# Kernel tuning notes

Hardware: AMD Instinct MI355X
Metric: run time of the kernel (lower is better)

## Reference

```python
import jax, jax.numpy as jnp
import numpy as np


def _d2(a, b):
    # squared euclidean distances, clamped at 0 (matches _full_cdist before sqrt)
    a2 = jnp.sum(a * a, axis=1)[:, None]
    b2 = jnp.sum(b * b, axis=1)[None, :]
    return jnp.clip(a2 + b2 - 2.0 * (a @ b.T), 0.0, None)


def _node_weights(pts, w1, b1, w2, b2):
    h = jax.nn.relu(pts @ w1 + b1)
    logits = h @ w2 + b2
    w = jax.nn.softplus(logits) + 1e-6
    w = w / jnp.sum(w)
    return w[:, 0]


def setup_inputs() -> dict:
    key = jax.random.key(0)
    ks = jax.random.split(key, 8)
    N, M, D, H, S = 8192, 8192, 2, 32, 3
    return {
        "base_points": jax.random.normal(ks[0], (N, D), jnp.float32),
        "target_points": jax.random.normal(ks[1], (M, D), jnp.float32),
        "log_sigmas": jnp.log(jnp.array([0.05, 0.1, 0.2], jnp.float32)),
        "log_scale": 0.1 * jax.random.normal(ks[2], (D,), jnp.float32),
        "wn_w1": jax.random.normal(ks[3], (D, H), jnp.float32) / np.sqrt(D),
        "wn_b1": jnp.zeros((H,), jnp.float32),
        "wn_w2": jax.random.normal(ks[4], (H, 1), jnp.float32) / np.sqrt(H),
        "wn_b2": jnp.zeros((1,), jnp.float32),
        "g_w1": jax.random.normal(ks[5], (4, H), jnp.float32) / 2.0,
        "g_b1": jnp.zeros((H,), jnp.float32),
        "g_w2": jax.random.normal(ks[6], (H, S), jnp.float32) / np.sqrt(H),
        "g_b2": jnp.zeros((S,), jnp.float32),
        "bias": jnp.zeros((1,), jnp.float32),
    }


def reference(base_points, target_points, log_sigmas, log_scale,
              wn_w1, wn_b1, wn_w2, wn_b2,
              g_w1, g_b1, g_w2, g_b2, bias):
    # learned anisotropic per-axis scale
    scale = jnp.exp(log_scale)
    base = base_points * scale
    target = target_points * scale

    # learned positive, normalized node weights (shared weight_net)
    w_b = _node_weights(base, wn_w1, wn_b1, wn_w2, wn_b2)
    w_t = _node_weights(target, wn_w1, wn_b1, wn_w2, wn_b2)

    # kde_mmd_loss with center=True: subtract weighted mean of each cloud.
    bc = base - jnp.sum(w_b[:, None] * base, axis=0)
    tc = target - jnp.sum(w_t[:, None] * target, axis=0)

    # squared distances computed ONCE, reused across all sigma bands
    d2_aa = _d2(bc, bc)
    d2_bb = _d2(tc, tc)
    d2_ab = _d2(bc, tc)

    sigmas = jnp.exp(log_sigmas)

    def band_loss(sigma):
        inv = 1.0 / (2.0 * sigma * sigma)
        kaa = jnp.exp(-d2_aa * inv)
        kbb = jnp.exp(-d2_bb * inv)
        kab = jnp.exp(-d2_ab * inv)
        # weighted MMD^2: w_a K_aa w_a + w_b K_bb w_b - 2 w_a K_ab w_b
        return (w_b @ (kaa @ w_b) + w_t @ (kbb @ w_t)
                - 2.0 * (w_b @ (kab @ w_t)))

    per_band = jnp.stack([band_loss(sigmas[i]) for i in range(sigmas.shape[0])])

    # gating statistics (torch.tensor([...]) detaches -> stop_gradient)
    dist = jnp.sqrt(_d2(base, target))
    mean_dist = jnp.mean(dist)
    var_dist = jnp.var(dist, ddof=1)  # torch .var() is unbiased
    n_base = base_points.shape[0]
    size_diff = abs(float(n_base - target_points.shape[0])) / (n_base + 1e-6)
    weight_var = jnp.var(w_b, ddof=1) + jnp.var(w_t, ddof=1)
    stats = jax.lax.stop_gradient(
        jnp.stack([mean_dist, var_dist,
                   jnp.asarray(size_diff, base.dtype), weight_var]))

    mix_logits = jax.nn.relu(stats @ g_w1 + g_b1) @ g_w2 + g_b2
    gw = jax.nn.softplus(mix_logits)
    gw = gw / jnp.sum(gw)
    return jnp.sum(gw * per_band) + bias[0]
```

## Files before the change

kernel.cpp:

```cpp
#include <hip/hip_runtime.h>
#include <math.h>

#define JTA 32
#define JTT 64
#define ITILE 1024
#define T8 8
#define NJOB_AB 2048
#define NJOB_TRI 576
#define NBLK (NJOB_AB + 2 * NJOB_TRI)
#define L2E 1.4426950408889634f

typedef float v2f __attribute__((ext_vector_type(2)));

__device__ inline float fexp2n(float x) {
  float r;
  asm("v_exp_f32 %0, -%1" : "=v"(r) : "v"(x));
  return r;
}
__device__ inline float fsqrt(float x) {
  float r;
  asm("v_sqrt_f32 %0, %1" : "=v"(r) : "v"(x));
  return r;
}

__device__ inline double wred_d(double v) {
#pragma unroll
  for (int o = 32; o > 0; o >>= 1) v += __shfl_down(v, o, 64);
  return v;
}

__device__ inline double bred(double v, double* sm) {
  v = wred_d(v);
  __syncthreads();
  if ((threadIdx.x & 63) == 0) sm[threadIdx.x >> 6] = v;
  __syncthreads();
  return sm[0] + sm[1] + sm[2] + sm[3];
}

__device__ inline void slot_reduce(const double* slot, double* smean, int nc) {
  if (threadIdx.x < 64) {
    int l = threadIdx.x;
    const double* sl = slot + l * 8;
    for (int c = 0; c < nc; ++c) {
      double v = sl[c];
      double vb = (l < 32) ? v : 0.0;
      double vt = (l < 32) ? 0.0 : v;
      vb = wred_d(vb);
      vt = wred_d(vt);
      if (l == 0) {
        smean[c] = vb;
        smean[8 + c] = vt;
      }
    }
  }
}

__global__ __launch_bounds__(256) void prep_kernel(
    const float* __restrict__ base, const float* __restrict__ target,
    const float* __restrict__ log_sigmas, const float* __restrict__ log_scale,
    const float* __restrict__ w1, const float* __restrict__ b1,
    const float* __restrict__ w2, const float* __restrict__ b2,
    float2* __restrict__ pxy, float* __restrict__ pu,
    double* __restrict__ slot, unsigned* __restrict__ fctr, int n) {
  __shared__ double sm[4];
  int gid = blockIdx.x * 256 + threadIdx.x;
  int isT = gid >= n;
  const float* pts = isT ? target : base;
  int idx = isT ? gid - n : gid;
  float ex = __expf(log_scale[0]);
  float ey = __expf(log_scale[1]);
  float s2 = __expf(log_sigmas[2]);
  float r2 = __fsqrt_rn(L2E / (2.f * s2 * s2));
  float2 p = ((const float2*)pts)[idx];
  float xr = p.x * ex, yr = p.y * ey;
  float logit = b2[0];
#pragma unroll
  for (int k = 0; k < 32; ++k) {
    float h = fmaf(xr, w1[k], fmaf(yr, w1[32 + k], b1[k]));
    h = fmaxf(h, 0.f);
    logit = fmaf(h, w2[k], logit);
  }
  float u = fmaxf(logit, 0.f) + log1pf(__expf(-fabsf(logit))) + 1e-6f;
  float X = xr * r2, Y = yr * r2;
  pxy[gid] = make_float2(X, Y);
  pu[gid] = u;
  double su = bred((double)u, sm);
  double qu = bred((double)u * (double)u, sm);
  double mx = bred((double)u * (double)X, sm);
  double my = bred((double)u * (double)Y, sm);
  double sx = bred((double)X, sm);
  double sy = bred((double)Y, sm);
  double sr = bred((double)X * (double)X + (double)Y * (double)Y, sm);
  if (threadIdx.x == 0) {
    double* s = slot + blockIdx.x * 8;
    s[0] = su;
    s[1] = qu;
    s[2] = mx;
    s[3] = my;
    s[4] = sx;
    s[5] = sy;
    s[6] = sr;
    s[7] = 0.0;
    if (blockIdx.x == 0) *fctr = 0u;
  }
}

template <bool AB, bool FAST>
__device__ inline void tile_loop(const float* sx, const float* sy,
                                 const float* su, const float* snb,
                                 const v2f xi2[4], const v2f yi2[4],
                                 const v2f al2[4], float rr0, float rr1,
                                 v2f a0[4], v2f a1[4], v2f a2[4], float& sdo) {
  constexpr int N2 = (AB ? JTA : JTT) / 2;
  float sda = 0.f, sdb = 0.f;
  const v2f vz = {0.f, 0.f};
#pragma unroll 2
  for (int jj = 0; jj < N2; ++jj) {
    v2f xj = *(const v2f*)&sx[2 * jj];
    v2f yj = *(const v2f*)&sy[2 * jj];
    v2f uj = *(const v2f*)&su[2 * jj];
    v2f nbj;
    if constexpr (AB) nbj = *(const v2f*)&snb[2 * jj];
#pragma unroll
    for (int i = 0; i < 4; ++i) {
      v2f dx = xi2[i] - xj;
      v2f dy = yi2[i] - yj;
      v2f pos = dx * dx + dy * dy;
      v2f k2 = {fexp2n(pos.x), fexp2n(pos.y)};
      v2f k0, k1;
      if constexpr (FAST) {
        v2f t = k2 * k2;
        k1 = t * t;
        v2f t1 = k1 * k1;
        k0 = t1 * t1;
      } else {
        v2f m1 = pos * rr1;
        v2f m0 = pos * rr0;
        k1 = {fexp2n(m1.x), fexp2n(m1.y)};
        k0 = {fexp2n(m0.x), fexp2n(m0.y)};
      }
      a0[i] += uj * k0;
      a1[i] += uj * k1;
      a2[i] += uj * k2;
      if constexpr (AB) {
        v2f anb = al2[i] + nbj;
        v2f d2u = pos + anb;
        d2u = __builtin_elementwise_max(d2u, vz);
        sda += fsqrt(d2u.x);
        sdb += fsqrt(d2u.y);
      }
    }
  }
  sdo = sda + sdb;
}

__global__ __launch_bounds__(256) void pair_kernel(
    const float2* __restrict__ pxy, const float* __restrict__ pu,
    const double* __restrict__ slot, double* __restrict__ paa,
    double* __restrict__ pbb, double* __restrict__ pab,
    double* __restrict__ psd, unsigned* __restrict__ fctr,
    const float* __restrict__ log_sigmas, const float* __restrict__ g_w1,
    const float* __restrict__ g_b1, const float* __restrict__ g_w2,
    const float* __restrict__ g_b2, const float* __restrict__ bias,
    float* __restrict__ out, int n) {
  __shared__ __align__(16) float sx[JTT];
  __shared__ __align__(16) float sy[JTT];
  __shared__ __align__(16) float su[JTT];
  __shared__ __align__(16) float snb[JTT];
  __shared__ double sm[4];
  __shared__ double smean[16];
  __shared__ int lastf;

  int b = blockIdx.x;
  int m, it, jt = 0, j0, pidx;
  if (b < NJOB_AB) {
    m = 2;
    pidx = b;
    it = b >> 8;
    j0 = (b & 255) * JTA;
  } else {
    int r = b - NJOB_AB;
    m = (r < NJOB_TRI) ? 0 : 1;
    if (m == 1) r -= NJOB_TRI;
    pidx = r;
    int tile = r >> 4;
    int q = r & 15;
    int idx = tile, len = T8;
    it = 0;
    while (idx >= len) {
      idx -= len;
      --len;
      ++it;
    }
    jt = it + idx;
    j0 = jt * ITILE + q * JTT;
  }
  const float2* pxyI = pxy + ((m == 1) ? n : 0);
  const float* puI = pu + ((m == 1) ? n : 0);
  const float2* pxyJ = pxy + ((m == 0) ? 0 : n);
  const float* puJ = pu + ((m == 0) ? 0 : n);

  float cx = 0.f, cy = 0.f, cx2 = 0.f, cy2 = 0.f, cc = 0.f;
  if (m == 2) {
    slot_reduce(slot, smean, 4);
  }

  float s0 = __expf(log_sigmas[0]);
  float s1 = __expf(log_sigmas[1]);
  float s2 = __expf(log_sigmas[2]);
  float rr0 = (s2 * s2) / (s0 * s0);
  float rr1 = (s2 * s2) / (s1 * s1);
  bool fast = (fabsf(rr0 - 16.f) <= 0.016f) && (fabsf(rr1 - 4.f) <= 0.004f);

  if (m == 2) {
    __syncthreads();
    cx = (float)(smean[2] / smean[0] - smean[10] / smean[8]);
    cy = (float)(smean[3] / smean[0] - smean[11] / smean[8]);
    cx2 = 2.f * cx;
    cy2 = 2.f * cy;
    cc = cx * cx + cy * cy;
  }

  int jcnt = (m == 2) ? JTA : JTT;
  if (threadIdx.x < jcnt) {
    float2 v = pxyJ[j0 + threadIdx.x];
    sx[threadIdx.x] = v.x;
    sy[threadIdx.x] = v.y;
    su[threadIdx.x] = puJ[j0 + threadIdx.x];
    if (m == 2) snb[threadIdx.x] = -fmaf(cx2, v.x, cy2 * v.y);
  }
  __syncthreads();

  int i0 = it * ITILE + threadIdx.x;
  v2f xi2[4], yi2[4], al2[4];
  float u[4];
#pragma unroll
  for (int i = 0; i < 4; ++i) {
    float2 P = pxyI[i0 + i * 256];
    u[i] = puI[i0 + i * 256];
    float xv = P.x, yv = P.y, alv = 0.f;
    if (m == 2) {
      xv -= cx;
      yv -= cy;
      alv = fmaf(cx2, xv, cy2 * yv) + cc;
    }
    xi2[i] = (v2f){xv, xv};
    yi2[i] = (v2f){yv, yv};
    al2[i] = (v2f){alv, alv};
  }

  v2f a0[4] = {}, a1[4] = {}, a2[4] = {};
  float sd = 0.f;
  if (m == 2) {
    if (fast)
      tile_loop<true, true>(sx, sy, su, snb, xi2, yi2, al2, rr0, rr1, a0, a1,
                            a2, sd);
    else
      tile_loop<true, false>(sx, sy, su, snb, xi2, yi2, al2, rr0, rr1, a0, a1,
                             a2, sd);
  } else {
    if (fast)
      tile_loop<false, true>(sx, sy, su, snb, xi2, yi2, al2, rr0, rr1, a0, a1,
                             a2, sd);
    else
      tile_loop<false, false>(sx, sy, su, snb, xi2, yi2, al2, rr0, rr1, a0,
                              a1, a2, sd);
  }

  double wgt = (m != 2 && jt != it) ? 2.0 : 1.0;
  double c0 = 0.0, c1 = 0.0, c2 = 0.0;
#pragma unroll
  for (int i = 0; i < 4; ++i) {
    c0 += (double)u[i] * (double)(a0[i].x + a0[i].y);
    c1 += (double)u[i] * (double)(a1[i].x + a1[i].y);
    c2 += (double)u[i] * (double)(a2[i].x + a2[i].y);
  }
  double r0 = bred(c0, sm) * wgt;
  double r1 = bred(c1, sm) * wgt;
  double r2d = bred(c2, sm) * wgt;
  double* prow = (m == 0) ? paa : (m == 1) ? pbb : pab;
  int stride = (m == 2) ? NJOB_AB : NJOB_TRI;
  if (threadIdx.x == 0) {
    prow[0 * stride + pidx] = r0;
    prow[1 * stride + pidx] = r1;
    prow[2 * stride + pidx] = r2d;
  }
  if (m == 2) {
    double rsd = bred((double)sd, sm);
    if (threadIdx.x == 0) psd[pidx] = rsd;
  }

  if (threadIdx.x == 0) {
    __threadfence();
    unsigned old = atomicAdd(fctr, 1u);
    lastf = (old == NBLK - 1) ? 1 : 0;
  }
  __syncthreads();
  if (!lastf) return;
  __threadfence();

  slot_reduce(slot, smean, 7);
  __syncthreads();
  int t = threadIdx.x;
  double vaa[3], vbb[3], vab[3];
  for (int s = 0; s < 3; ++s) {
    const double* pa = paa + s * NJOB_TRI;
    const double* pb = pbb + s * NJOB_TRI;
    const double* pc = pab + s * NJOB_AB;
    double va = pa[t] + pa[t + 256] + ((t < 64) ? pa[t + 512] : 0.0);
    double vb = pb[t] + pb[t + 256] + ((t < 64) ? pb[t + 512] : 0.0);
    double vc = 0.0;
#pragma unroll
    for (int qq = 0; qq < 8; ++qq) vc += pc[t + 256 * qq];
    vaa[s] = bred(va, sm);
    vbb[s] = bred(vb, sm);
    vab[s] = bred(vc, sm);
  }
  double sdv = 0.0;
#pragma unroll
  for (int qq = 0; qq < 8; ++qq) sdv += psd[t + 256 * qq];
  double sdt = bred(sdv, sm);

  if (threadIdx.x == 0) {
    double Sb = smean[0], Qb = smean[1], St = smean[8], Qt = smean[9];
    double SXb = smean[4], SYb = smean[5], SRb = smean[6];
    double SXt = smean[12], SYt = smean[13], SRt = smean[14];
    double pband[3];
    for (int s = 0; s < 3; ++s)
      pband[s] = vaa[s] / (Sb * Sb) + vbb[s] / (St * St) -
                 2.0 * vab[s] / (Sb * St);
    double NN = (double)n;
    double sq_sc = NN * (SRb + SRt) - 2.0 * (SXb * SXt + SYb * SYt);
    double s2d = (double)s2;
    double r2sq = (double)L2E / (2.0 * s2d * s2d);
    double sd_real = sdt / sqrt(r2sq);
    double sq_real = sq_sc / r2sq;
    double NM = NN * NN;
    double mean_d = sd_real / NM;
    double var_d = (sq_real - sd_real * sd_real / NM) / (NM - 1.0);
    double wv = (Qb / (Sb * Sb) - 1.0 / NN) / (NN - 1.0) +
                (Qt / (St * St) - 1.0 / NN) / (NN - 1.0);
    float st[4] = {(float)mean_d, (float)var_d, 0.f, (float)wv};
    float gl[3] = {g_b2[0], g_b2[1], g_b2[2]};
    for (int k = 0; k < 32; ++k) {
      float h = g_b1[k];
      for (int c = 0; c < 4; ++c) h = fmaf(st[c], g_w1[c * 32 + k], h);
      h = fmaxf(h, 0.f);
      for (int s = 0; s < 3; ++s) gl[s] = fmaf(h, g_w2[k * 3 + s], gl[s]);
    }
    float gw[3];
    float gsum = 0.f;
    for (int s = 0; s < 3; ++s) {
      gw[s] = fmaxf(gl[s], 0.f) + log1pf(__expf(-fabsf(gl[s])));
      gsum += gw[s];
    }
    double r = 0.0;
    for (int s = 0; s < 3; ++s) r += (double)(gw[s] / gsum) * pband[s];
    out[0] = (float)(r + (double)bias[0]);
  }
}

extern "C" void kernel_launch(void* const* d_in, const int* in_sizes, int n_in,
                              void* d_out, int out_size, void* d_ws,
                              size_t ws_size, hipStream_t stream) {
  const float* base = (const float*)d_in[0];
  const float* target = (const float*)d_in[1];
  const float* log_sigmas = (const float*)d_in[2];
  const float* log_scale = (const float*)d_in[3];
  const float* wn_w1 = (const float*)d_in[4];
  const float* wn_b1 = (const float*)d_in[5];
  const float* wn_w2 = (const float*)d_in[6];
  const float* wn_b2 = (const float*)d_in[7];
  const float* g_w1 = (const float*)d_in[8];
  const float* g_b1 = (const float*)d_in[9];
  const float* g_w2 = (const float*)d_in[10];
  const float* g_b2 = (const float*)d_in[11];
  const float* bias = (const float*)d_in[12];
  int n = in_sizes[0] / 2;

  double* dbase = (double*)d_ws;
  double* slot = dbase;
  double* paa = dbase + 512;
  double* pbb = paa + 3 * NJOB_TRI;
  double* pab = pbb + 3 * NJOB_TRI;
  double* psd = pab + 3 * NJOB_AB;
  double* dend = psd + NJOB_AB;
  float2* pxy = (float2*)dend;
  float* pu = (float*)(pxy + 2 * n);
  unsigned* fctr = (unsigned*)(pu + 2 * n);

  prep_kernel<<<(2 * n) / 256, 256, 0, stream>>>(
      base, target, log_sigmas, log_scale, wn_w1, wn_b1, wn_w2, wn_b2, pxy, pu,
      slot, fctr, n);
  pair_kernel<<<NBLK, 256, 0, stream>>>(pxy, pu, slot, paa, pbb, pab, psd,
                                        fctr, log_sigmas, g_w1, g_b1, g_w2,
                                        g_b2, bias, (float*)d_out, n);
}
```

Baseline: 166.0 us.

## Use persistent blocks with atomic work queue and per-block accumulated partials

Replaces the one-job-per-block launch with a fixed grid of persistent blocks that pull jobs from an atomic counter, and widens cross-tile jobs to 64 columns so they match the triangular jobs. Each block keeps scaled running sums across its jobs and writes one set of partials, which simplifies the final reduction. This aims to even out load imbalance and cut per-block reduction and launch overhead. The cost is an atomic plus a barrier per job and every block doing the slot reduction up front.

```diff
diff --git a/kernel.cpp b/kernel.cpp
--- a/kernel.cpp
+++ b/kernel.cpp
@@ -1,13 +1,13 @@
 #include <hip/hip_runtime.h>
 #include <math.h>
 
-#define JTA 32
-#define JTT 64
+#define JT 64
 #define ITILE 1024
 #define T8 8
-#define NJOB_AB 2048
+#define NJOB_AB 1024
 #define NJOB_TRI 576
-#define NBLK (NJOB_AB + 2 * NJOB_TRI)
+#define NJOB (NJOB_AB + 2 * NJOB_TRI)
+#define GRID 2048
 #define L2E 1.4426950408889634f
 
 typedef float v2f __attribute__((ext_vector_type(2)));
@@ -61,7 +61,8 @@
     const float* __restrict__ w1, const float* __restrict__ b1,
     const float* __restrict__ w2, const float* __restrict__ b2,
     float2* __restrict__ pxy, float* __restrict__ pu,
-    double* __restrict__ slot, unsigned* __restrict__ fctr, int n) {
+    double* __restrict__ slot, unsigned* __restrict__ fctr,
+    unsigned* __restrict__ qctr, int n) {
   __shared__ double sm[4];
   int gid = blockIdx.x * 256 + threadIdx.x;
   int isT = gid >= n;
@@ -101,7 +102,10 @@
     s[5] = sy;
     s[6] = sr;
     s[7] = 0.0;
-    if (blockIdx.x == 0) *fctr = 0u;
+    if (blockIdx.x == 0) {
+      *fctr = 0u;
+      *qctr = 0u;
+    }
   }
 }
 
@@ -111,11 +115,10 @@
                                  const v2f xi2[4], const v2f yi2[4],
                                  const v2f al2[4], float rr0, float rr1,
                                  v2f a0[4], v2f a1[4], v2f a2[4], float& sdo) {
-  constexpr int N2 = (AB ? JTA : JTT) / 2;
   float sda = 0.f, sdb = 0.f;
   const v2f vz = {0.f, 0.f};
 #pragma unroll 2
-  for (int jj = 0; jj < N2; ++jj) {
+  for (int jj = 0; jj < JT / 2; ++jj) {
     v2f xj = *(const v2f*)&sx[2 * jj];
     v2f yj = *(const v2f*)&sy[2 * jj];
     v2f uj = *(const v2f*)&su[2 * jj];
@@ -156,54 +159,31 @@
 
 __global__ __launch_bounds__(256) void pair_kernel(
     const float2* __restrict__ pxy, const float* __restrict__ pu,
-    const double* __restrict__ slot, double* __restrict__ paa,
-    double* __restrict__ pbb, double* __restrict__ pab,
-    double* __restrict__ psd, unsigned* __restrict__ fctr,
+    const double* __restrict__ slot, double* __restrict__ pblk,
+    unsigned* __restrict__ fctr, unsigned* __restrict__ qctr,
     const float* __restrict__ log_sigmas, const float* __restrict__ g_w1,
     const float* __restrict__ g_b1, const float* __restrict__ g_w2,
     const float* __restrict__ g_b2, const float* __restrict__ bias,
     float* __restrict__ out, int n) {
-  __shared__ __align__(16) float sx[JTT];
-  __shared__ __align__(16) float sy[JTT];
-  __shared__ __align__(16) float su[JTT];
-  __shared__ __align__(16) float snb[JTT];
+  __shared__ __align__(16) float sx[JT];
+  __shared__ __align__(16) float sy[JT];
+  __shared__ __align__(16) float su[JT];
+  __shared__ __align__(16) float snb[JT];
   __shared__ double sm[4];
   __shared__ double smean[16];
+  __shared__ int sjob;
   __shared__ int lastf;
 
-  int b = blockIdx.x;
-  int m, it, jt = 0, j0, pidx;
-  if (b < NJOB_AB) {
-    m = 2;
-    pidx = b;
-    it = b >> 8;
-    j0 = (b & 255) * JTA;
-  } else {
-    int r = b - NJOB_AB;
-    m = (r < NJOB_TRI) ? 0 : 1;
-    if (m == 1) r -= NJOB_TRI;
-    pidx = r;
-    int tile = r >> 4;
-    int q = r & 15;
-    int idx = tile, len = T8;
-    it = 0;
-    while (idx >= len) {
-      idx -= len;
-      --len;
-      ++it;
-    }
-    jt = it + idx;
-    j0 = jt * ITILE + q * JTT;
-  }
-  const float2* pxyI = pxy + ((m == 1) ? n : 0);
-  const float* puI = pu + ((m == 1) ? n : 0);
-  const float2* pxyJ = pxy + ((m == 0) ? 0 : n);
-  const float* puJ = pu + ((m == 0) ? 0 : n);
-
-  float cx = 0.f, cy = 0.f, cx2 = 0.f, cy2 = 0.f, cc = 0.f;
-  if (m == 2) {
-    slot_reduce(slot, smean, 4);
-  }
+  slot_reduce(slot, smean, 4);
+  __syncthreads();
+  double Sb = smean[0], St = smean[8];
+  float cx = (float)(smean[2] / Sb - smean[10] / St);
+  float cy = (float)(smean[3] / Sb - smean[11] / St);
+  float cx2 = 2.f * cx, cy2 = 2.f * cy;
+  float cc = cx * cx + cy * cy;
+  double sc_aa = 1.0 / (Sb * Sb);
+  double sc_bb = 1.0 / (St * St);
+  double sc_ab = -2.0 / (Sb * St);
 
   float s0 = __expf(log_sigmas[0]);
   float s1 = __expf(log_sigmas[1]);
@@ -212,88 +192,116 @@
   float rr1 = (s2 * s2) / (s1 * s1);
   bool fast = (fabsf(rr0 - 16.f) <= 0.016f) && (fabsf(rr1 - 4.f) <= 0.004f);
 
-  if (m == 2) {
+  double cacc0 = 0.0, cacc1 = 0.0, cacc2 = 0.0, sdacc = 0.0;
+  for (;;) {
+    if (threadIdx.x == 0) sjob = (int)atomicAdd(qctr, 1u);
     __syncthreads();
-    cx = (float)(smean[2] / smean[0] - smean[10] / smean[8]);
-    cy = (float)(smean[3] / smean[0] - smean[11] / smean[8]);
-    cx2 = 2.f * cx;
-    cy2 = 2.f * cy;
-    cc = cx * cx + cy * cy;
-  }
-
-  int jcnt = (m == 2) ? JTA : JTT;
-  if (threadIdx.x < jcnt) {
-    float2 v = pxyJ[j0 + threadIdx.x];
-    sx[threadIdx.x] = v.x;
-    sy[threadIdx.x] = v.y;
-    su[threadIdx.x] = puJ[j0 + threadIdx.x];
-    if (m == 2) snb[threadIdx.x] = -fmaf(cx2, v.x, cy2 * v.y);
-  }
-  __syncthreads();
-
-  int i0 = it * ITILE + threadIdx.x;
-  v2f xi2[4], yi2[4], al2[4];
-  float u[4];
-#pragma unroll
-  for (int i = 0; i < 4; ++i) {
-    float2 P = pxyI[i0 + i * 256];
-    u[i] = puI[i0 + i * 256];
-    float xv = P.x, yv = P.y, alv = 0.f;
+    int jb = sjob;
+    if (jb >= NJOB) break;
+
+    int m, it, jt = 0, j0;
+    double wgt = 1.0;
+    if (jb < NJOB_AB) {
+      m = 2;
+      it = jb >> 7;
+      j0 = (jb & 127) * JT;
+    } else {
+      int r = jb - NJOB_AB;
+      m = (r < NJOB_TRI) ? 0 : 1;
+      if (m == 1) r -= NJOB_TRI;
+      int tile = r >> 4;
+      int q = r & 15;
+      int idx = tile, len = T8;
+      it = 0;
+      while (idx >= len) {
+        idx -= len;
+        --len;
+        ++it;
+      }
+      jt = it + idx;
+      j0 = jt * ITILE + q * JT;
+      if (jt != it) wgt = 2.0;
+    }
+    const float2* pxyI = pxy + ((m == 1) ? n : 0);
+    const float* puI = pu + ((m == 1) ? n : 0);
+    const float2* pxyJ = pxy + ((m == 0) ? 0 : n);
+    const float* puJ = pu + ((m == 0) ? 0 : n);
+
+    if (threadIdx.x < JT) {
+      float2 v = pxyJ[j0 + threadIdx.x];
+      sx[threadIdx.x] = v.x;
+      sy[threadIdx.x] = v.y;
+      su[threadIdx.x] = puJ[j0 + threadIdx.x];
+      if (m == 2) snb[threadIdx.x] = -fmaf(cx2, v.x, cy2 * v.y);
+    }
+
+    int i0 = it * ITILE + threadIdx.x;
+    v2f xi2[4], yi2[4], al2[4];
+    float u[4];
+#pragma unroll
+    for (int i = 0; i < 4; ++i) {
+      float2 P = pxyI[i0 + i * 256];
+      u[i] = puI[i0 + i * 256];
+      float xv = P.x, yv = P.y, alv = 0.f;
+      if (m == 2) {
+        xv -= cx;
+        yv -= cy;
+        alv = fmaf(cx2, xv, cy2 * yv) + cc;
+      }
+      xi2[i] = (v2f){xv, xv};
+      yi2[i] = (v2f){yv, yv};
+      al2[i] = (v2f){alv, alv};
+    }
+    __syncthreads();
+
+    v2f a0[4] = {}, a1[4] = {}, a2[4] = {};
+    float sd = 0.f;
     if (m == 2) {
-      xv -= cx;
-      yv -= cy;
-      alv = fmaf(cx2, xv, cy2 * yv) + cc;
-    }
-    xi2[i] = (v2f){xv, xv};
-    yi2[i] = (v2f){yv, yv};
-    al2[i] = (v2f){alv, alv};
-  }
-
-  v2f a0[4] = {}, a1[4] = {}, a2[4] = {};
-  float sd = 0.f;
-  if (m == 2) {
-    if (fast)
-      tile_loop<true, true>(sx, sy, su, snb, xi2, yi2, al2, rr0, rr1, a0, a1,
-                            a2, sd);
-    else
-      tile_loop<true, false>(sx, sy, su, snb, xi2, yi2, al2, rr0, rr1, a0, a1,
-                             a2, sd);
-  } else {
-    if (fast)
-      tile_loop<false, true>(sx, sy, su, snb, xi2, yi2, al2, rr0, rr1, a0, a1,
-                             a2, sd);
-    else
-      tile_loop<false, false>(sx, sy, su, snb, xi2, yi2, al2, rr0, rr1, a0,
-                              a1, a2, sd);
-  }
-
-  double wgt = (m != 2 && jt != it) ? 2.0 : 1.0;
-  double c0 = 0.0, c1 = 0.0, c2 = 0.0;
-#pragma unroll
-  for (int i = 0; i < 4; ++i) {
-    c0 += (double)u[i] * (double)(a0[i].x + a0[i].y);
-    c1 += (double)u[i] * (double)(a1[i].x + a1[i].y);
-    c2 += (double)u[i] * (double)(a2[i].x + a2[i].y);
-  }
-  double r0 = bred(c0, sm) * wgt;
-  double r1 = bred(c1, sm) * wgt;
-  double r2d = bred(c2, sm) * wgt;
-  double* prow = (m == 0) ? paa : (m == 1) ? pbb : pab;
-  int stride = (m == 2) ? NJOB_AB : NJOB_TRI;
+      if (fast)
+        tile_loop<true, true>(sx, sy, su, snb, xi2, yi2, al2, rr0, rr1, a0, a1,
+                              a2, sd);
+      else
+        tile_loop<true, false>(sx, sy, su, snb, xi2, yi2, al2, rr0, rr1, a0,
+                               a1, a2, sd);
+    } else {
+      if (fast)
+        tile_loop<false, true>(sx, sy, su, snb, xi2, yi2, al2, rr0, rr1, a0,
+                               a1, a2, sd);
+      else
+        tile_loop<false, false>(sx, sy, su, snb, xi2, yi2, al2, rr0, rr1, a0,
+                                a1, a2, sd);
+    }
+
+    double jc0 = 0.0, jc1 = 0.0, jc2 = 0.0;
+#pragma unroll
+    for (int i = 0; i < 4; ++i) {
+      jc0 += (double)u[i] * (double)(a0[i].x + a0[i].y);
+      jc1 += (double)u[i] * (double)(a1[i].x + a1[i].y);
+      jc2 += (double)u[i] * (double)(a2[i].x + a2[i].y);
+    }
+    double jscale = ((m == 0) ? sc_aa : (m == 1) ? sc_bb : sc_ab) * wgt;
+    cacc0 += jscale * jc0;
+    cacc1 += jscale * jc1;
+    cacc2 += jscale * jc2;
+    if (m == 2) sdacc += (double)sd;
+  }
+
+  double r0 = bred(cacc0, sm);
+  double r1 = bred(cacc1, sm);
+  double r2d = bred(cacc2, sm);
+  double rsd = bred(sdacc, sm);
   if (threadIdx.x == 0) {
-    prow[0 * stride + pidx] = r0;
-    prow[1 * stride + pidx] = r1;
-    prow[2 * stride + pidx] = r2d;
-  }
-  if (m == 2) {
-    double rsd = bred((double)sd, sm);
-    if (threadIdx.x == 0) psd[pidx] = rsd;
+    double* p = pblk + (size_t)blockIdx.x * 4;
+    p[0] = r0;
+    p[1] = r1;
+    p[2] = r2d;
+    p[3] = rsd;
   }
 
   if (threadIdx.x == 0) {
     __threadfence();
     unsigned old = atomicAdd(fctr, 1u);
-    lastf = (old == NBLK - 1) ? 1 : 0;
+    lastf = (old == GRID - 1) ? 1 : 0;
   }
   __syncthreads();
   if (!lastf) return;
@@ -302,44 +310,36 @@
   slot_reduce(slot, smean, 7);
   __syncthreads();
   int t = threadIdx.x;
-  double vaa[3], vbb[3], vab[3];
-  for (int s = 0; s < 3; ++s) {
-    const double* pa = paa + s * NJOB_TRI;
-    const double* pb = pbb + s * NJOB_TRI;
-    const double* pc = pab + s * NJOB_AB;
-    double va = pa[t] + pa[t + 256] + ((t < 64) ? pa[t + 512] : 0.0);
-    double vb = pb[t] + pb[t + 256] + ((t < 64) ? pb[t + 512] : 0.0);
-    double vc = 0.0;
-#pragma unroll
-    for (int qq = 0; qq < 8; ++qq) vc += pc[t + 256 * qq];
-    vaa[s] = bred(va, sm);
-    vbb[s] = bred(vb, sm);
-    vab[s] = bred(vc, sm);
-  }
-  double sdv = 0.0;
-#pragma unroll
-  for (int qq = 0; qq < 8; ++qq) sdv += psd[t + 256 * qq];
-  double sdt = bred(sdv, sm);
+  double v0 = 0.0, v1 = 0.0, v2 = 0.0, vs = 0.0;
+#pragma unroll
+  for (int q = 0; q < GRID / 256; ++q) {
+    const double* p = pblk + (size_t)(t + 256 * q) * 4;
+    v0 += p[0];
+    v1 += p[1];
+    v2 += p[2];
+    vs += p[3];
+  }
+  v0 = bred(v0, sm);
+  v1 = bred(v1, sm);
+  v2 = bred(v2, sm);
+  vs = bred(vs, sm);
 
   if (threadIdx.x == 0) {
-    double Sb = smean[0], Qb = smean[1], St = smean[8], Qt = smean[9];
+    double Sb2 = smean[0], Qb = smean[1], St2 = smean[8], Qt = smean[9];
     double SXb = smean[4], SYb = smean[5], SRb = smean[6];
     double SXt = smean[12], SYt = smean[13], SRt = smean[14];
-    double pband[3];
-    for (int s = 0; s < 3; ++s)
-      pband[s] = vaa[s] / (Sb * Sb) + vbb[s] / (St * St) -
-                 2.0 * vab[s] / (Sb * St);
+    double pband[3] = {v0, v1, v2};
     double NN = (double)n;
     double sq_sc = NN * (SRb + SRt) - 2.0 * (SXb * SXt + SYb * SYt);
     double s2d = (double)s2;
     double r2sq = (double)L2E / (2.0 * s2d * s2d);
-    double sd_real = sdt / sqrt(r2sq);
+    double sd_real = vs / sqrt(r2sq);
     double sq_real = sq_sc / r2sq;
     double NM = NN * NN;
     double mean_d = sd_real / NM;
     double var_d = (sq_real - sd_real * sd_real / NM) / (NM - 1.0);
-    double wv = (Qb / (Sb * Sb) - 1.0 / NN) / (NN - 1.0) +
-                (Qt / (St * St) - 1.0 / NN) / (NN - 1.0);
+    double wv = (Qb / (Sb2 * Sb2) - 1.0 / NN) / (NN - 1.0) +
+                (Qt / (St2 * St2) - 1.0 / NN) / (NN - 1.0);
     float st[4] = {(float)mean_d, (float)var_d, 0.f, (float)wv};
     float gl[3] = {g_b2[0], g_b2[1], g_b2[2]};
     for (int k = 0; k < 32; ++k) {
@@ -380,19 +380,17 @@
 
   double* dbase = (double*)d_ws;
   double* slot = dbase;
-  double* paa = dbase + 512;
-  double* pbb = paa + 3 * NJOB_TRI;
-  double* pab = pbb + 3 * NJOB_TRI;
-  double* psd = pab + 3 * NJOB_AB;
-  double* dend = psd + NJOB_AB;
+  double* pblk = dbase + 512;
+  double* dend = pblk + GRID * 4;
   float2* pxy = (float2*)dend;
   float* pu = (float*)(pxy + 2 * n);
   unsigned* fctr = (unsigned*)(pu + 2 * n);
+  unsigned* qctr = fctr + 1;
 
   prep_kernel<<<(2 * n) / 256, 256, 0, stream>>>(
       base, target, log_sigmas, log_scale, wn_w1, wn_b1, wn_w2, wn_b2, pxy, pu,
-      slot, fctr, n);
-  pair_kernel<<<NBLK, 256, 0, stream>>>(pxy, pu, slot, paa, pbb, pab, psd,
-                                        fctr, log_sigmas, g_w1, g_b1, g_w2,
-                                        g_b2, bias, (float*)d_out, n);
-}
+      slot, fctr, qctr, n);
+  pair_kernel<<<GRID, 256, 0, stream>>>(pxy, pu, slot, pblk, fctr, qctr,
+                                        log_sigmas, g_w1, g_b1, g_w2, g_b2,
+                                        bias, (float*)d_out, n);
+}
```

Measured after the change: 181.0 us. 1.09x slower.

## Expand squared distance into dot form, widen AB tiles, batch block reductions

Applied to the files above, without the earlier changes.

The pair loop now writes the squared distance as -2*xi·xj + |xj|^2 + |xi|^2. The per-point norms are precomputed, one into shared memory and one held in registers, so each pair costs two FMAs plus an add instead of two subtracts and squares. The cross (AB) job tile is widened from 32 to 64 columns, which halves the number of AB blocks and the partial sums the final block has to gather. The four per-block reductions are fused into one pass of wavefront reductions and a single barrier instead of four serialized block reductions. The expanded distance form can lose accuracy through cancellation for nearby points, and fewer AB blocks means less parallelism.

```diff
diff --git a/kernel.cpp b/kernel.cpp
--- a/kernel.cpp
+++ b/kernel.cpp
@@ -1,11 +1,10 @@
 #include <hip/hip_runtime.h>
 #include <math.h>
 
-#define JTA 32
-#define JTT 64
+#define JT 64
 #define ITILE 1024
 #define T8 8
-#define NJOB_AB 2048
+#define NJOB_AB 1024
 #define NJOB_TRI 576
 #define NBLK (NJOB_AB + 2 * NJOB_TRI)
 #define L2E 1.4426950408889634f
@@ -107,25 +106,24 @@
 
 template <bool AB, bool FAST>
 __device__ inline void tile_loop(const float* sx, const float* sy,
-                                 const float* su, const float* snb,
-                                 const v2f xi2[4], const v2f yi2[4],
-                                 const v2f al2[4], float rr0, float rr1,
-                                 v2f a0[4], v2f a1[4], v2f a2[4], float& sdo) {
-  constexpr int N2 = (AB ? JTA : JTT) / 2;
-  float sda = 0.f, sdb = 0.f;
+                                 const float* sr, const float* su,
+                                 const float* snb, const v2f xin2[4],
+                                 const v2f yin2[4], const v2f ric2[4],
+                                 const v2f rca2[4], float rr0, float rr1,
+                                 v2f a0[4], v2f a1[4], v2f a2[4], v2f& sdv) {
   const v2f vz = {0.f, 0.f};
 #pragma unroll 2
-  for (int jj = 0; jj < N2; ++jj) {
+  for (int jj = 0; jj < JT / 2; ++jj) {
     v2f xj = *(const v2f*)&sx[2 * jj];
     v2f yj = *(const v2f*)&sy[2 * jj];
+    v2f rj = *(const v2f*)&sr[2 * jj];
     v2f uj = *(const v2f*)&su[2 * jj];
     v2f nbj;
     if constexpr (AB) nbj = *(const v2f*)&snb[2 * jj];
 #pragma unroll
     for (int i = 0; i < 4; ++i) {
-      v2f dx = xi2[i] - xj;
-      v2f dy = yi2[i] - yj;
-      v2f pos = dx * dx + dy * dy;
+      v2f core = xin2[i] * xj + (yin2[i] * yj + rj);
+      v2f pos = core + ric2[i];
       v2f k2 = {fexp2n(pos.x), fexp2n(pos.y)};
       v2f k0, k1;
       if constexpr (FAST) {
@@ -143,15 +141,13 @@
       a1[i] += uj * k1;
       a2[i] += uj * k2;
       if constexpr (AB) {
-        v2f anb = al2[i] + nbj;
-        v2f d2u = pos + anb;
+        v2f d2u = core + (rca2[i] + nbj);
         d2u = __builtin_elementwise_max(d2u, vz);
-        sda += fsqrt(d2u.x);
-        sdb += fsqrt(d2u.y);
+        v2f s = {fsqrt(d2u.x), fsqrt(d2u.y)};
+        sdv += s;
       }
     }
   }
-  sdo = sda + sdb;
 }
 
 __global__ __launch_bounds__(256) void pair_kernel(
@@ -163,11 +159,13 @@
     const float* __restrict__ g_b1, const float* __restrict__ g_w2,
     const float* __restrict__ g_b2, const float* __restrict__ bias,
     float* __restrict__ out, int n) {
-  __shared__ __align__(16) float sx[JTT];
-  __shared__ __align__(16) float sy[JTT];
-  __shared__ __align__(16) float su[JTT];
-  __shared__ __align__(16) float snb[JTT];
+  __shared__ __align__(16) float sx[JT];
+  __shared__ __align__(16) float sy[JT];
+  __shared__ __align__(16) float sr[JT];
+  __shared__ __align__(16) float su[JT];
+  __shared__ __align__(16) float snb[JT];
   __shared__ double sm[4];
+  __shared__ double smq[16];
   __shared__ double smean[16];
   __shared__ int lastf;
 
@@ -176,8 +174,8 @@
   if (b < NJOB_AB) {
     m = 2;
     pidx = b;
-    it = b >> 8;
-    j0 = (b & 255) * JTA;
+    it = b >> 7;
+    j0 = (b & 127) * JT;
   } else {
     int r = b - NJOB_AB;
     m = (r < NJOB_TRI) ? 0 : 1;
@@ -193,7 +191,7 @@
       ++it;
     }
     jt = it + idx;
-    j0 = jt * ITILE + q * JTT;
+    j0 = jt * ITILE + q * JT;
   }
   const float2* pxyI = pxy + ((m == 1) ? n : 0);
   const float* puI = pu + ((m == 1) ? n : 0);
@@ -221,18 +219,18 @@
     cc = cx * cx + cy * cy;
   }
 
-  int jcnt = (m == 2) ? JTA : JTT;
-  if (threadIdx.x < jcnt) {
+  if (threadIdx.x < JT) {
     float2 v = pxyJ[j0 + threadIdx.x];
     sx[threadIdx.x] = v.x;
     sy[threadIdx.x] = v.y;
+    sr[threadIdx.x] = fmaf(v.x, v.x, v.y * v.y);
     su[threadIdx.x] = puJ[j0 + threadIdx.x];
     if (m == 2) snb[threadIdx.x] = -fmaf(cx2, v.x, cy2 * v.y);
   }
   __syncthreads();
 
   int i0 = it * ITILE + threadIdx.x;
-  v2f xi2[4], yi2[4], al2[4];
+  v2f xin2[4], yin2[4], ric2[4], rca2[4];
   float u[4];
 #pragma unroll
   for (int i = 0; i < 4; ++i) {
@@ -244,30 +242,31 @@
       yv -= cy;
       alv = fmaf(cx2, xv, cy2 * yv) + cc;
     }
-    xi2[i] = (v2f){xv, xv};
-    yi2[i] = (v2f){yv, yv};
-    al2[i] = (v2f){alv, alv};
+    float ric = fmaf(xv, xv, yv * yv);
+    xin2[i] = (v2f){-2.f * xv, -2.f * xv};
+    yin2[i] = (v2f){-2.f * yv, -2.f * yv};
+    ric2[i] = (v2f){ric, ric};
+    rca2[i] = (v2f){ric + alv, ric + alv};
   }
 
   v2f a0[4] = {}, a1[4] = {}, a2[4] = {};
-  float sd = 0.f;
+  v2f sdv = {0.f, 0.f};
   if (m == 2) {
     if (fast)
-      tile_loop<true, true>(sx, sy, su, snb, xi2, yi2, al2, rr0, rr1, a0, a1,
-                            a2, sd);
+      tile_loop<true, true>(sx, sy, sr, su, snb, xin2, yin2, ric2, rca2, rr0,
+                            rr1, a0, a1, a2, sdv);
     else
-      tile_loop<true, false>(sx, sy, su, snb, xi2, yi2, al2, rr0, rr1, a0, a1,
-                             a2, sd);
+      tile_loop<true, false>(sx, sy, sr, su, snb, xin2, yin2, ric2, rca2, rr0,
+                             rr1, a0, a1, a2, sdv);
   } else {
     if (fast)
-      tile_loop<false, true>(sx, sy, su, snb, xi2, yi2, al2, rr0, rr1, a0, a1,
-                             a2, sd);
+      tile_loop<false, true>(sx, sy, sr, su, snb, xin2, yin2, ric2, rca2, rr0,
+                             rr1, a0, a1, a2, sdv);
     else
-      tile_loop<false, false>(sx, sy, su, snb, xi2, yi2, al2, rr0, rr1, a0,
-                              a1, a2, sd);
-  }
-
-  double wgt = (m != 2 && jt != it) ? 2.0 : 1.0;
+      tile_loop<false, false>(sx, sy, sr, su, snb, xin2, yin2, ric2, rca2, rr0,
+                              rr1, a0, a1, a2, sdv);
+  }
+
   double c0 = 0.0, c1 = 0.0, c2 = 0.0;
 #pragma unroll
   for (int i = 0; i < 4; ++i) {
@@ -275,19 +274,31 @@
     c1 += (double)u[i] * (double)(a1[i].x + a1[i].y);
     c2 += (double)u[i] * (double)(a2[i].x + a2[i].y);
   }
-  double r0 = bred(c0, sm) * wgt;
-  double r1 = bred(c1, sm) * wgt;
-  double r2d = bred(c2, sm) * wgt;
-  double* prow = (m == 0) ? paa : (m == 1) ? pbb : pab;
-  int stride = (m == 2) ? NJOB_AB : NJOB_TRI;
+  double sdd = (double)(sdv.x + sdv.y);
+  c0 = wred_d(c0);
+  c1 = wred_d(c1);
+  c2 = wred_d(c2);
+  sdd = wred_d(sdd);
+  if ((threadIdx.x & 63) == 0) {
+    double* q = &smq[(threadIdx.x >> 6) * 4];
+    q[0] = c0;
+    q[1] = c1;
+    q[2] = c2;
+    q[3] = sdd;
+  }
+  __syncthreads();
   if (threadIdx.x == 0) {
-    prow[0 * stride + pidx] = r0;
-    prow[1 * stride + pidx] = r1;
-    prow[2 * stride + pidx] = r2d;
-  }
-  if (m == 2) {
-    double rsd = bred((double)sd, sm);
-    if (threadIdx.x == 0) psd[pidx] = rsd;
+    double wgt = (m != 2 && jt != it) ? 2.0 : 1.0;
+    double t0 = smq[0] + smq[4] + smq[8] + smq[12];
+    double t1 = smq[1] + smq[5] + smq[9] + smq[13];
+    double t2 = smq[2] + smq[6] + smq[10] + smq[14];
+    double ts = smq[3] + smq[7] + smq[11] + smq[15];
+    double* prow = (m == 0) ? paa : (m == 1) ? pbb : pab;
+    int stride = (m == 2) ? NJOB_AB : NJOB_TRI;
+    prow[0 * stride + pidx] = t0 * wgt;
+    prow[1 * stride + pidx] = t1 * wgt;
+    prow[2 * stride + pidx] = t2 * wgt;
+    if (m == 2) psd[pidx] = ts;
   }
 
   if (threadIdx.x == 0) {
@@ -309,17 +320,13 @@
     const double* pc = pab + s * NJOB_AB;
     double va = pa[t] + pa[t + 256] + ((t < 64) ? pa[t + 512] : 0.0);
     double vb = pb[t] + pb[t + 256] + ((t < 64) ? pb[t + 512] : 0.0);
-    double vc = 0.0;
-#pragma unroll
-    for (int qq = 0; qq < 8; ++qq) vc += pc[t + 256 * qq];
+    double vc = pc[t] + pc[t + 256] + pc[t + 512] + pc[t + 768];
     vaa[s] = bred(va, sm);
     vbb[s] = bred(vb, sm);
     vab[s] = bred(vc, sm);
   }
-  double sdv = 0.0;
-#pragma unroll
-  for (int qq = 0; qq < 8; ++qq) sdv += psd[t + 256 * qq];
-  double sdt = bred(sdv, sm);
+  double sdg = psd[t] + psd[t + 256] + psd[t + 512] + psd[t + 768];
+  double sdt = bred(sdg, sm);
 
   if (threadIdx.x == 0) {
     double Sb = smean[0], Qb = smean[1], St = smean[8], Qt = smean[9];
```

Measured after the change: 147.0 us, median of 2. 11.5% less time.
